# Kernel optimization log

Hardware: AMD Instinct MI355X
Metric: run time of the kernel (lower is better)

The kernel has to match this reference:

```python
import jax, jax.numpy as jnp
import numpy as np

B, T, IN = 8, 1000, 80
CONV = 256
CCEP = 222            # ltv_out_channels
FFT_SIZE = 1024
HOP = 256
WIN = 2 * HOP         # 512
PAD = (FFT_SIZE - CCEP) // 2   # 401
NFFT = 2048


def _conv1d_same(x, W, b, groups):
    # x: (B,T,C); W: (O, C//groups, 3); equivalent to torch Conv1d pad=2 then [1:-1]
    y = jax.lax.conv_general_dilated(
        jnp.transpose(x, (0, 2, 1)), W, (1,), [(1, 1)],
        feature_group_count=groups,
        dimension_numbers=('NCH', 'OIH', 'NCH'))
    return jnp.transpose(y, (0, 2, 1)) + b


def _forward(x, z, W1, b1, W2, b2, W3, b3, W4, b4):
    Bx, Tx, _ = x.shape
    # ---- ConvLayers ----
    h = jax.nn.relu(_conv1d_same(x, W1, b1, 1))
    h = jax.nn.relu(_conv1d_same(h, W2, b2, 8))
    h = jax.nn.relu(_conv1d_same(h, W3, b3, 8))
    ccep = _conv1d_same(h, W4, b4, 1)            # (B,T,222)
    q = jnp.arange(1, CCEP // 2 + 1, dtype=x.dtype)
    quef = jnp.concatenate([q[::-1], q])          # [111..1,1..111]
    ccep = ccep / quef
    # ---- ccep -> impulse (log-magnitude cepstrum -> minimum-ish phase impulse) ----
    c = jnp.pad(ccep, ((0, 0), (0, 0), (PAD, PAD)))           # (B,T,1024)
    Y = jnp.fft.fft(c, n=FFT_SIZE, axis=-1)
    mag = jnp.power(10.0, Y.real)
    imp = jnp.fft.ifft(mag * jnp.exp(1j * Y.imag), n=FFT_SIZE, axis=-1).real  # (B,T,1024)
    # ---- time-varying impulse convolution (cross-correlation per frame) ----
    L = z.shape[-1]
    zz = z.reshape(Bx, 1, L)
    zp = jnp.pad(zz, ((0, 0), (0, 0), (WIN // 2 - 1, WIN // 2)))
    starts = jnp.arange(Tx) * HOP
    frames = zp[:, :, starts[:, None] + jnp.arange(WIN)]       # (B,1,T,512)
    fp = jnp.pad(frames, ((0, 0), (0, 0), (0, 0), (FFT_SIZE // 2 - 1, FFT_SIZE // 2)))  # len 1535
    # corr[s] = sum_k fp[s+k] * imp[k], s in [0,512); linear corr via zero-padded FFT
    Fz = jnp.fft.rfft(fp, n=NFFT, axis=-1)                     # (B,1,T,NFFT//2+1)
    Fy = jnp.fft.rfft(imp, n=NFFT, axis=-1)[:, None]           # (B,1,T,NFFT//2+1)
    corr = jnp.fft.irfft(Fz * jnp.conj(Fy), n=NFFT, axis=-1)[..., :WIN]  # (B,1,T,512)
    # ---- overlap-add ----
    n = jnp.arange(WIN, dtype=x.dtype)
    win = 0.5 * (1.0 - jnp.cos(2.0 * jnp.pi * n / WIN))        # periodic hann, win_norm=1
    zw = corr * win
    l, r = zw[..., :HOP], zw[..., HOP:]
    out = l + jnp.roll(r, 1, axis=2)
    return out.reshape(Bx, 1, Tx * HOP)


def setup_inputs() -> dict:
    key = jax.random.key(0)
    ks = jax.random.split(key, 12)
    x = jax.random.normal(ks[0], (B, T, IN), dtype=jnp.float32)
    z = jax.random.normal(ks[1], (B, 1, T * HOP), dtype=jnp.float32)
    def w(k, o, i, kk, scale):
        return jax.random.normal(k, (o, i, kk), dtype=jnp.float32) * (scale / np.sqrt(i * kk))
    W1 = w(ks[2], CONV, IN, 3, 1.0)
    b1 = jnp.zeros((CONV,), jnp.float32)
    W2 = w(ks[3], CONV, CONV // 8, 3, 1.0)
    b2 = jnp.zeros((CONV,), jnp.float32)
    W3 = w(ks[4], CONV, CONV // 8, 3, 1.0)
    b3 = jnp.zeros((CONV,), jnp.float32)
    W4 = w(ks[5], CCEP, CONV, 3, 0.01)   # small scale keeps 10**(.) well-conditioned
    b4 = jnp.zeros((CCEP,), jnp.float32)
    return {"x": x, "z": z, "W1": W1, "b1": b1, "W2": W2, "b2": b2,
            "W3": W3, "b3": b3, "W4": W4, "b4": b4}


def reference(x, z, W1, b1, W2, b2, W3, b3, W4, b4):
    return _forward(x, z, W1, b1, W2, b2, W3, b3, W4, b4)
```

## Files before the change

kernel.cpp:

```cpp
#include <hip/hip_runtime.h>
#include <hip/hip_bf16.h>

#define T_LEN 1000
#define B_N 8
#define IN_CH 80
#define CONV_CH 256
#define CCEP_N 222

typedef short s8v __attribute__((ext_vector_type(8)));
typedef float f16v __attribute__((ext_vector_type(16)));

#define TWO_PI 6.28318530717958647692f

__global__ __launch_bounds__(256) void k_prep(
    const float* __restrict__ W1, const float* __restrict__ W2,
    const float* __restrict__ W3, const float* __restrict__ W4,
    float* __restrict__ Wt1, float* __restrict__ Wt2, float* __restrict__ Wt3,
    __hip_bfloat16* __restrict__ Wc, float2* __restrict__ twTab,
    float* __restrict__ winTab) {
  const int bid = blockIdx.x, tid = threadIdx.x;
  if (bid < 240) {
    int e = bid * 256 + tid;
    int o = e / 240, k = e - o * 240;
    Wt1[k * 256 + o] = W1[e];
  } else if (bid < 336) {
    int e = (bid - 240) * 256 + tid;
    int o = e / 96, k = e - o * 96;
    Wt2[k * 256 + o] = W2[e];
  } else if (bid < 432) {
    int e = (bid - 336) * 256 + tid;
    int o = e / 96, k = e - o * 96;
    Wt3[k * 256 + o] = W3[e];
  } else if (bid < 1200) {
    int e = (bid - 432) * 256 + tid;
    int kloc = e & 31, n = (e >> 5) & 255, chg = e >> 13;
    int kp = chg * 32 + kloc;
    int kappa = kp >> 8, i = kp & 255;
    float v = 0.f;
    if (n < CCEP_N) {
      float invq = 1.f / (float)((n < 111) ? (111 - n) : (n - 110));
      v = W4[n * 768 + i * 3 + kappa] * invq;
    }
    Wc[e] = __float2bfloat16(v);
  } else {
    int e = (bid - 1200) * 256 + tid;
    if (e < 1020) {
      int Q, off;
      if (e < 768)       { Q = 256; off = 0; }
      else if (e < 960)  { Q = 64;  off = 768; }
      else if (e < 1008) { Q = 16;  off = 960; }
      else               { Q = 4;   off = 1008; }
      int rem = e - off;
      int r = rem / Q, pos = rem - r * Q;
      float ang = (TWO_PI * (float)((r + 1) * pos)) / (float)(4 * Q);
      float s, c;
      sincosf(ang, &s, &c);
      twTab[e] = make_float2(c, s);
    } else if (e < 1532) {
      int n = e - 1020;
      winTab[n] = (0.5f - 0.5f * cosf(TWO_PI * (float)n / 512.f)) * (1.f / 1024.f);
    }
  }
}

__global__ __launch_bounds__(256) void k_conv1t(const float* __restrict__ x,
    const float* __restrict__ Wt, const float* __restrict__ bias,
    float* __restrict__ out) {
  const int b = blockIdx.y;
  const int t0 = blockIdx.x * 10;
  const int o = threadIdx.x;
  __shared__ float hs[IN_CH * 14];
  for (int e = threadIdx.x; e < 12 * IN_CH; e += 256) {
    int r = e / IN_CH, c = e - r * IN_CH;
    int t = t0 - 1 + r;
    hs[c * 14 + r] = (t >= 0 && t < T_LEN) ? x[(b * T_LEN + t) * IN_CH + c] : 0.f;
  }
  __syncthreads();
  float acc[10];
  float bv = bias[o];
#pragma unroll
  for (int j = 0; j < 10; j++) acc[j] = bv;
  for (int i = 0; i < IN_CH; i++) {
    float w0 = Wt[(3 * i + 0) * 256 + o];
    float w1 = Wt[(3 * i + 1) * 256 + o];
    float w2 = Wt[(3 * i + 2) * 256 + o];
    const float* row = &hs[i * 14];
    float a[12];
#pragma unroll
    for (int u = 0; u < 6; u++) *(float2*)&a[2 * u] = *(const float2*)(row + 2 * u);
#pragma unroll
    for (int j = 0; j < 10; j++) {
      acc[j] = fmaf(a[j], w0, acc[j]);
      acc[j] = fmaf(a[j + 1], w1, acc[j]);
      acc[j] = fmaf(a[j + 2], w2, acc[j]);
    }
  }
#pragma unroll
  for (int j = 0; j < 10; j++)
    out[(b * T_LEN + t0 + j) * CONV_CH + o] = fmaxf(acc[j], 0.f);
}

__global__ __launch_bounds__(256) void k_convg2(const float* __restrict__ h,
    const float* __restrict__ Wt2, const float* __restrict__ b2,
    const float* __restrict__ Wt3, const float* __restrict__ b3,
    __hip_bfloat16* __restrict__ out) {
  const int b = blockIdx.y;
  const int t0 = blockIdx.x * 10;
  const int o = threadIdx.x;
  const int cb = (o >> 5) << 5;
  __shared__ float hs1[CONV_CH * 14];
  __shared__ float hs2[CONV_CH * 14];
  for (int e = threadIdx.x; e < 14 * CONV_CH; e += 256) {
    int r = e >> 8, c = e & 255;
    int t = t0 - 2 + r;
    hs1[c * 14 + r] = (t >= 0 && t < T_LEN) ? h[(b * T_LEN + t) * CONV_CH + c] : 0.f;
  }
  __syncthreads();
  {
    float acc[12];
    float bv = b2[o];
#pragma unroll
    for (int j = 0; j < 12; j++) acc[j] = bv;
    for (int i = 0; i < 32; i++) {
      float w0 = Wt2[(3 * i + 0) * 256 + o];
      float w1 = Wt2[(3 * i + 1) * 256 + o];
      float w2 = Wt2[(3 * i + 2) * 256 + o];
      const float* row = &hs1[(cb + i) * 14];
      float a[14];
#pragma unroll
      for (int u = 0; u < 7; u++) *(float2*)&a[2 * u] = *(const float2*)(row + 2 * u);
#pragma unroll
      for (int j = 0; j < 12; j++) {
        acc[j] = fmaf(a[j], w0, acc[j]);
        acc[j] = fmaf(a[j + 1], w1, acc[j]);
        acc[j] = fmaf(a[j + 2], w2, acc[j]);
      }
    }
#pragma unroll
    for (int j = 0; j < 12; j++) {
      int t = t0 - 1 + j;
      hs2[o * 14 + j] = (t >= 0 && t < T_LEN) ? fmaxf(acc[j], 0.f) : 0.f;
    }
  }
  __syncthreads();
  {
    float acc[10];
    float bv = b3[o];
#pragma unroll
    for (int j = 0; j < 10; j++) acc[j] = bv;
    for (int i = 0; i < 32; i++) {
      float w0 = Wt3[(3 * i + 0) * 256 + o];
      float w1 = Wt3[(3 * i + 1) * 256 + o];
      float w2 = Wt3[(3 * i + 2) * 256 + o];
      const float* row = &hs2[(cb + i) * 14];
      float a[12];
#pragma unroll
      for (int u = 0; u < 6; u++) *(float2*)&a[2 * u] = *(const float2*)(row + 2 * u);
#pragma unroll
      for (int j = 0; j < 10; j++) {
        acc[j] = fmaf(a[j], w0, acc[j]);
        acc[j] = fmaf(a[j + 1], w1, acc[j]);
        acc[j] = fmaf(a[j + 2], w2, acc[j]);
      }
    }
#pragma unroll
    for (int j = 0; j < 10; j++)
      out[(b * T_LEN + t0 + j) * CONV_CH + o] = __float2bfloat16(fmaxf(acc[j], 0.f));
  }
}

#define APITCH 264
#define BPITCH 40
#define PSTRIDE 1792000
__global__ __launch_bounds__(256) void k_conv4m(
    const __hip_bfloat16* __restrict__ h3, const __hip_bfloat16* __restrict__ Wc,
    const float* __restrict__ bias, float* __restrict__ Pbase) {
  const int mb = blockIdx.x, b = blockIdx.y, ks = blockIdx.z;
  float* __restrict__ P = Pbase + (size_t)ks * PSTRIDE;
  const int t0 = mb * 64;
  const int tid = threadIdx.x;
  const int w = tid >> 6, lane = tid & 63;
  const int wm = w >> 1, wn = w & 1;
  const int lm = lane & 31, half = lane >> 5;

  __shared__ short h3s[67 * APITCH];
  __shared__ short Bs[2][256 * BPITCH];

  const ushort* h3u = (const ushort*)h3;
  for (int g = tid; g < 67 * 64; g += 256) {
    int rr = g >> 6, c4 = g & 63;
    int t = t0 + rr - 1;
    uint2 v = make_uint2(0u, 0u);
    if (t >= 0 && t < T_LEN)
      v = *(const uint2*)(h3u + (b * T_LEN + t) * CONV_CH + c4 * 4);
    *(uint2*)(h3s + rr * APITCH + c4 * 4) = v;
  }

  const ushort* Wu = (const ushort*)(Wc) + (size_t)(ks * 6) * 8192;
#pragma unroll
  for (int it = 0; it < 4; ++it) {
    int idx = (it * 256 + tid) * 8;
    uint4 v = *(const uint4*)(Wu + idx);
    int n = idx >> 5, kloc = idx & 31;
    *(uint4*)(Bs[0] + n * BPITCH + kloc) = v;
  }
  __syncthreads();

  f16v acc0 = {}, acc1 = {}, acc2 = {}, acc3 = {};

  for (int ch = 0; ch < 6; ++ch) {
    const int p = ch & 1;
    if (ch < 5) {
      const ushort* src = Wu + (ch + 1) * 8192;
#pragma unroll
      for (int it = 0; it < 4; ++it) {
        int idx = (it * 256 + tid) * 8;
        uint4 v = *(const uint4*)(src + idx);
        int n = idx >> 5, kloc = idx & 31;
        *(uint4*)(Bs[p ^ 1] + n * BPITCH + kloc) = v;
      }
    }
#pragma unroll
    for (int s = 0; s < 2; ++s) {
      int k0 = ks * 192 + ch * 32 + s * 16;
      int kappa = k0 >> 8, i0 = k0 & 255;
      s8v a = *(const s8v*)(h3s + (wm * 32 + lm + kappa) * APITCH + i0 + half * 8);
      const short* bp = Bs[p] + (wn * 128 + lm) * BPITCH + s * 16 + half * 8;
      s8v b0 = *(const s8v*)(bp);
      s8v b1 = *(const s8v*)(bp + 32 * BPITCH);
      s8v b2 = *(const s8v*)(bp + 64 * BPITCH);
      s8v b3 = *(const s8v*)(bp + 96 * BPITCH);
      acc0 = __builtin_amdgcn_mfma_f32_32x32x16_bf16(a, b0, acc0, 0, 0, 0);
      acc1 = __builtin_amdgcn_mfma_f32_32x32x16_bf16(a, b1, acc1, 0, 0, 0);
      acc2 = __builtin_amdgcn_mfma_f32_32x32x16_bf16(a, b2, acc2, 0, 0, 0);
      acc3 = __builtin_amdgcn_mfma_f32_32x32x16_bf16(a, b3, acc3, 0, 0, 0);
    }
    __syncthreads();
  }

  const int col = lm;
#pragma unroll
  for (int nt = 0; nt < 4; ++nt) {
    int c = wn * 128 + nt * 32 + col;
    if (c >= CCEP_N) continue;
    float bq = 0.f;
    if (ks == 0) {
      float invq = 1.f / (float)((c < 111) ? (111 - c) : (c - 110));
      bq = bias[c] * invq;
    }
    const f16v* A = (nt == 0) ? &acc0 : (nt == 1) ? &acc1 : (nt == 2) ? &acc2 : &acc3;
#pragma unroll
    for (int reg = 0; reg < 16; ++reg) {
      int row = (reg & 3) + 8 * (reg >> 2) + 4 * half;
      int t = t0 + wm * 32 + row;
      if (t < T_LEN)
        P[(size_t)(b * T_LEN + t) * 224 + c] = (*A)[reg] + bq;
    }
  }
}

__device__ __forceinline__ float2 cmul(float2 a, float2 b) {
  return make_float2(fmaf(a.x, b.x, -(a.y * b.y)), fmaf(a.x, b.y, a.y * b.x));
}
__device__ __forceinline__ float2 cadd(float2 a, float2 b) { return make_float2(a.x + b.x, a.y + b.y); }
__device__ __forceinline__ float2 csub(float2 a, float2 b) { return make_float2(a.x - b.x, a.y - b.y); }

#define LIDX(i) ((i) + ((i) >> 2))

template <int Q, int OFF>
__device__ __forceinline__ void fwd_stage2(float2* __restrict__ A,
    float2* __restrict__ B, const float2* __restrict__ Tw, int j) {
  const int pos = j & (Q - 1);
  const int base = ((j - pos) << 2) + pos;
  float2 e1 = Tw[OFF + pos], e2 = Tw[OFF + Q + pos], e3 = Tw[OFF + 2 * Q + pos];
  const float2 w1 = make_float2(e1.x, -e1.y);
  const float2 w2 = make_float2(e2.x, -e2.y);
  const float2 w3 = make_float2(e3.x, -e3.y);
#pragma unroll
  for (int arr = 0; arr < 2; ++arr) {
    float2* X = arr ? B : A;
    float2 a = X[LIDX(base)], b = X[LIDX(base + Q)];
    float2 cc = X[LIDX(base + 2 * Q)], d = X[LIDX(base + 3 * Q)];
    float2 t0 = cadd(a, cc), t1 = csub(a, cc), t2 = cadd(b, d), bd = csub(b, d);
    float2 t3 = make_float2(bd.y, -bd.x);
    X[LIDX(base)]         = cadd(t0, t2);
    X[LIDX(base + Q)]     = cmul(cadd(t1, t3), w1);
    X[LIDX(base + 2 * Q)] = cmul(csub(t0, t2), w2);
    X[LIDX(base + 3 * Q)] = cmul(csub(t1, t3), w3);
  }
}

template <int Q, int OFF>
__device__ __forceinline__ void inv_stage_t(float2* __restrict__ X,
    const float2* __restrict__ Tw, int j) {
  const int pos = j & (Q - 1);
  const int base = ((j - pos) << 2) + pos;
  const float2 w1 = Tw[OFF + pos];
  const float2 w2 = Tw[OFF + Q + pos];
  const float2 w3 = Tw[OFF + 2 * Q + pos];
  float2 a = X[LIDX(base)];
  float2 b = cmul(X[LIDX(base + Q)], w1);
  float2 cc = cmul(X[LIDX(base + 2 * Q)], w2);
  float2 d = cmul(X[LIDX(base + 3 * Q)], w3);
  float2 t0 = cadd(a, cc), t1 = csub(a, cc), t2 = cadd(b, d), bd = csub(b, d);
  float2 t3 = make_float2(-bd.y, bd.x);
  X[LIDX(base)]         = cadd(t0, t2);
  X[LIDX(base + Q)]     = cadd(t1, t3);
  X[LIDX(base + 2 * Q)] = csub(t0, t2);
  X[LIDX(base + 3 * Q)] = csub(t1, t3);
}

__device__ __forceinline__ int rev4d(int v) {
  return ((v & 3) << 6) | (((v >> 2) & 3) << 4) | (((v >> 4) & 3) << 2) | ((v >> 6) & 3);
}

__global__ __launch_bounds__(256) void k_fft(const float* __restrict__ Pb,
    const float* __restrict__ z, const float2* __restrict__ twg,
    const float* __restrict__ wing, float* __restrict__ out,
    float* __restrict__ sbl, float* __restrict__ sbr) {
  const int u = blockIdx.x, b = blockIdx.y;
  const int tA = 2 * u, tB = tA + 1;
  const int btA = b * T_LEN + tA, btB = btA + 1;
  const int j = threadIdx.x;
  __shared__ float2 WlA[1280];
  __shared__ float2 WlB[1280];
  __shared__ float2 Tws[1020];
  for (int e = j; e < 1020; e += 256) Tws[e] = twg[e];

  const float* zb = z + b * 256000;
  float f0A = 0.f, fS, f1B = 0.f;
  {
    int zi0 = tA * 256 + j - 255;
    f0A = (zi0 >= 0) ? zb[zi0] : 0.f;
    fS = zb[tA * 256 + j + 1];
    int zi2 = tB * 256 + j + 1;
    f1B = (zi2 < 256000) ? zb[zi2] : 0.f;
  }
  float c1A = 0.f, c2A = 0.f, c1B = 0.f, c2B = 0.f;
  if (j >= 145) {
    int mA = btA * 224 + (j - 145), mB = btB * 224 + (j - 145);
    c1A = (Pb[mA] + Pb[mA + PSTRIDE]) + (Pb[mA + 2 * PSTRIDE] + Pb[mA + 3 * PSTRIDE]);
    c1B = (Pb[mB] + Pb[mB + PSTRIDE]) + (Pb[mB + 2 * PSTRIDE] + Pb[mB + 3 * PSTRIDE]);
  }
  if (j < 111) {
    int mA = btA * 224 + (j + 111), mB = btB * 224 + (j + 111);
    c2A = (Pb[mA] + Pb[mA + PSTRIDE]) + (Pb[mA + 2 * PSTRIDE] + Pb[mA + 3 * PSTRIDE]);
    c2B = (Pb[mB] + Pb[mB + PSTRIDE]) + (Pb[mB + 2 * PSTRIDE] + Pb[mB + 3 * PSTRIDE]);
  }
  __syncthreads();

  {
    float2 e1 = Tws[j], e2 = Tws[256 + j], e3 = Tws[512 + j];
    const float2 w1 = make_float2(e1.x, -e1.y);
    const float2 w2 = make_float2(e2.x, -e2.y);
    const float2 w3 = make_float2(e3.x, -e3.y);
    {
      float2 t0 = make_float2(c2A, f0A);
      float2 t1 = make_float2(-c2A, f0A);
      float2 t2 = make_float2(c1A, fS);
      float2 t3 = make_float2(fS, -c1A);
      WlA[LIDX(j)]       = cadd(t0, t2);
      WlA[LIDX(j + 256)] = cmul(cadd(t1, t3), w1);
      WlA[LIDX(j + 512)] = cmul(csub(t0, t2), w2);
      WlA[LIDX(j + 768)] = cmul(csub(t1, t3), w3);
    }
    {
      float2 t0 = make_float2(c2B, fS);
      float2 t1 = make_float2(-c2B, fS);
      float2 t2 = make_float2(c1B, f1B);
      float2 t3 = make_float2(f1B, -c1B);
      WlB[LIDX(j)]       = cadd(t0, t2);
      WlB[LIDX(j + 256)] = cmul(cadd(t1, t3), w1);
      WlB[LIDX(j + 512)] = cmul(csub(t0, t2), w2);
      WlB[LIDX(j + 768)] = cmul(csub(t1, t3), w3);
    }
  }
  __syncthreads();

  fwd_stage2<64, 768>(WlA, WlB, Tws, j);  __syncthreads();
  fwd_stage2<16, 960>(WlA, WlB, Tws, j);  __syncthreads();
  fwd_stage2<4, 1008>(WlA, WlB, Tws, j);  __syncthreads();

  const int base = 4 * j;
  float2 XA[4], XB[4];
  {
    float2 u0 = WlA[LIDX(base)], u1 = WlA[LIDX(base + 1)];
    float2 u2 = WlA[LIDX(base + 2)], u3 = WlA[LIDX(base + 3)];
    float2 t0 = cadd(u0, u2), t1 = csub(u0, u2), t2 = cadd(u1, u3), bd = csub(u1, u3);
    float2 t3 = make_float2(bd.y, -bd.x);
    XA[0] = cadd(t0, t2); XA[1] = cadd(t1, t3); XA[2] = csub(t0, t2); XA[3] = csub(t1, t3);
  }
  {
    float2 u0 = WlB[LIDX(base)], u1 = WlB[LIDX(base + 1)];
    float2 u2 = WlB[LIDX(base + 2)], u3 = WlB[LIDX(base + 3)];
    float2 t0 = cadd(u0, u2), t1 = csub(u0, u2), t2 = cadd(u1, u3), bd = csub(u1, u3);
    float2 t3 = make_float2(bd.y, -bd.x);
    XB[0] = cadd(t0, t2); XB[1] = cadd(t1, t3); XB[2] = csub(t0, t2); XB[3] = csub(t1, t3);
  }
#pragma unroll
  for (int q = 0; q < 4; ++q) { WlA[LIDX(base + q)] = XA[q]; WlB[LIDX(base + q)] = XB[q]; }
  __syncthreads();

  const int r0 = rev4d(j);
  const bool self0 = (r0 == 0);
  const int jp = self0 ? 0 : rev4d((256 - r0) & 255);
  float2 PA[4], PB[4];
#pragma unroll
  for (int q = 0; q < 4; ++q) { PA[q] = WlA[LIDX(4 * jp + q)]; PB[q] = WlB[LIDX(4 * jp + q)]; }
  float2 Z[4];
#pragma unroll
  for (int q = 0; q < 4; ++q) {
    float2 SA, SB;
    {
      float2 A = XA[q];
      float2 Bc = self0 ? PA[(4 - q) & 3] : PA[3 - q];
      float2 Y = make_float2(0.5f * (A.x + Bc.x), 0.5f * (A.y - Bc.y));
      float2 F = make_float2(0.5f * (A.y + Bc.y), -0.5f * (A.x - Bc.x));
      float mag = __expf(Y.x * 2.30258509299404568402f);
      float sy, cy;
      __sincosf(Y.y, &sy, &cy);
      float gr = mag * cy, gi = mag * sy;
      SA = make_float2(fmaf(F.x, gr, F.y * gi), fmaf(F.x, gi, -(F.y * gr)));
    }
    {
      float2 A = XB[q];
      float2 Bc = self0 ? PB[(4 - q) & 3] : PB[3 - q];
      float2 Y = make_float2(0.5f * (A.x + Bc.x), 0.5f * (A.y - Bc.y));
      float2 F = make_float2(0.5f * (A.y + Bc.y), -0.5f * (A.x - Bc.x));
      float mag = __expf(Y.x * 2.30258509299404568402f);
      float sy, cy;
      __sincosf(Y.y, &sy, &cy);
      float gr = mag * cy, gi = mag * sy;
      SB = make_float2(fmaf(F.x, gr, F.y * gi), fmaf(F.x, gi, -(F.y * gr)));
    }
    Z[q] = make_float2(SA.x - SB.y, SA.y + SB.x);
  }
  __syncthreads();

  {
    float2 t0 = cadd(Z[0], Z[2]), t1 = csub(Z[0], Z[2]), t2 = cadd(Z[1], Z[3]), bd = csub(Z[1], Z[3]);
    float2 t3 = make_float2(-bd.y, bd.x);
    WlA[LIDX(base)]     = cadd(t0, t2);
    WlA[LIDX(base + 1)] = cadd(t1, t3);
    WlA[LIDX(base + 2)] = csub(t0, t2);
    WlA[LIDX(base + 3)] = csub(t1, t3);
  }
  __syncthreads();

  inv_stage_t<4, 1008>(WlA, Tws, j);  __syncthreads();
  inv_stage_t<16, 960>(WlA, Tws, j);  __syncthreads();
  inv_stage_t<64, 768>(WlA, Tws, j);  __syncthreads();

  {
    float2 w1 = Tws[j], w2 = Tws[256 + j], w3 = Tws[512 + j];
    float2 a = WlA[LIDX(j)];
    float2 bb = cmul(WlA[LIDX(j + 256)], w1);
    float2 cc = cmul(WlA[LIDX(j + 512)], w2);
    float2 d = cmul(WlA[LIDX(j + 768)], w3);
    float2 t0 = cadd(a, cc), t1 = csub(a, cc), t2 = cadd(bb, d), bd = csub(bb, d);
    float2 t3 = make_float2(-bd.y, bd.x);
    float2 Cj    = cadd(t0, t2);
    float2 Cj256 = cadd(t1, t3);
    int n1 = 511 - j, n2 = 255 - j;
    float wn1 = wing[n1], wn2 = wing[n2];
    float vA_l = Cj256.x * wn2;
    float vAB  = Cj.x * wn1 + Cj256.y * wn2;
    float vB_r = Cj.y * wn1;
    out[(b * T_LEN + tB) * 256 + n2] = vAB;
    int su = (b * 500 + u) * 256 + n2;
    sbl[su] = vA_l;
    sbr[su] = vB_r;
  }
}

__global__ __launch_bounds__(256) void k_even(const float* __restrict__ sbl,
    const float* __restrict__ sbr, float* __restrict__ out) {
  int idx = blockIdx.x * 256 + threadIdx.x;
  int n = idx & 255;
  int bu = idx >> 8;
  int u = bu % 500, b = bu / 500;
  int up = (u == 0) ? 499 : u - 1;
  out[(b * T_LEN + 2 * u) * 256 + n] = sbl[idx] + sbr[(b * 500 + up) * 256 + n];
}

extern "C" void kernel_launch(void* const* d_in, const int* in_sizes, int n_in,
                              void* d_out, int out_size, void* d_ws, size_t ws_size,
                              hipStream_t stream) {
  const float* x  = (const float*)d_in[0];
  const float* z  = (const float*)d_in[1];
  const float* W1 = (const float*)d_in[2];
  const float* b1 = (const float*)d_in[3];
  const float* W2 = (const float*)d_in[4];
  const float* b2 = (const float*)d_in[5];
  const float* W3 = (const float*)d_in[6];
  const float* b3 = (const float*)d_in[7];
  const float* W4 = (const float*)d_in[8];
  const float* b4 = (const float*)d_in[9];

  float* ws   = (float*)d_ws;
  float* bufA = ws;
  __hip_bfloat16* h3bf = (__hip_bfloat16*)(ws + 2048000);
  float* Pb   = ws + 3072000;
  float* sbl  = ws + 10240000;
  float* sbr  = ws + 11264000;
  float* Wt1  = ws + 12288000;
  float* Wt2  = ws + 12349440;
  float* Wt3  = ws + 12374016;
  __hip_bfloat16* Wc = (__hip_bfloat16*)(ws + 12398592);
  float2* twTab = (float2*)(ws + 12496896);
  float* winTab = ws + 12498944;
  float* out = (float*)d_out;

  dim3 blk(256);
  k_prep<<<1206, blk, 0, stream>>>(W1, W2, W3, W4, Wt1, Wt2, Wt3, Wc,
                                   twTab, winTab);

  dim3 cgrid10(T_LEN / 10, B_N);
  k_conv1t<<<cgrid10, blk, 0, stream>>>(x, Wt1, b1, bufA);
  k_convg2<<<cgrid10, blk, 0, stream>>>(bufA, Wt2, b2, Wt3, b3, h3bf);
  dim3 g4(16, B_N, 4);
  k_conv4m<<<g4, blk, 0, stream>>>(h3bf, Wc, b4, Pb);
  dim3 gf(T_LEN / 2, B_N);
  k_fft<<<gf, blk, 0, stream>>>(Pb, z, twTab, winTab, out, sbl, sbr);
  k_even<<<4000, blk, 0, stream>>>(sbl, sbr, out);
}
```

Measured before the change: 173.4 us.

## Fuse first convolution into grouped conv kernel with halo recompute

Merges the first dense conv layer into the kernel that runs the two grouped convs. Each block now loads a wider input window and recomputes conv1 for 14 time steps into shared memory. This removes the intermediate fp32 activation buffer's global write and read and one kernel launch. In exchange it adds redundant halo computation for conv1 and more shared memory per block.

```diff
diff --git a/kernel.cpp b/kernel.cpp
--- a/kernel.cpp
+++ b/kernel.cpp
@@ -63,44 +63,8 @@
   }
 }
 
-__global__ __launch_bounds__(256) void k_conv1t(const float* __restrict__ x,
-    const float* __restrict__ Wt, const float* __restrict__ bias,
-    float* __restrict__ out) {
-  const int b = blockIdx.y;
-  const int t0 = blockIdx.x * 10;
-  const int o = threadIdx.x;
-  __shared__ float hs[IN_CH * 14];
-  for (int e = threadIdx.x; e < 12 * IN_CH; e += 256) {
-    int r = e / IN_CH, c = e - r * IN_CH;
-    int t = t0 - 1 + r;
-    hs[c * 14 + r] = (t >= 0 && t < T_LEN) ? x[(b * T_LEN + t) * IN_CH + c] : 0.f;
-  }
-  __syncthreads();
-  float acc[10];
-  float bv = bias[o];
-#pragma unroll
-  for (int j = 0; j < 10; j++) acc[j] = bv;
-  for (int i = 0; i < IN_CH; i++) {
-    float w0 = Wt[(3 * i + 0) * 256 + o];
-    float w1 = Wt[(3 * i + 1) * 256 + o];
-    float w2 = Wt[(3 * i + 2) * 256 + o];
-    const float* row = &hs[i * 14];
-    float a[12];
-#pragma unroll
-    for (int u = 0; u < 6; u++) *(float2*)&a[2 * u] = *(const float2*)(row + 2 * u);
-#pragma unroll
-    for (int j = 0; j < 10; j++) {
-      acc[j] = fmaf(a[j], w0, acc[j]);
-      acc[j] = fmaf(a[j + 1], w1, acc[j]);
-      acc[j] = fmaf(a[j + 2], w2, acc[j]);
-    }
-  }
-#pragma unroll
-  for (int j = 0; j < 10; j++)
-    out[(b * T_LEN + t0 + j) * CONV_CH + o] = fmaxf(acc[j], 0.f);
-}
-
-__global__ __launch_bounds__(256) void k_convg2(const float* __restrict__ h,
+__global__ __launch_bounds__(256) void k_convall(const float* __restrict__ x,
+    const float* __restrict__ Wt1, const float* __restrict__ b1,
     const float* __restrict__ Wt2, const float* __restrict__ b2,
     const float* __restrict__ Wt3, const float* __restrict__ b3,
     __hip_bfloat16* __restrict__ out) {
@@ -108,12 +72,40 @@
   const int t0 = blockIdx.x * 10;
   const int o = threadIdx.x;
   const int cb = (o >> 5) << 5;
+  __shared__ float xs[IN_CH * 18];
   __shared__ float hs1[CONV_CH * 14];
   __shared__ float hs2[CONV_CH * 14];
-  for (int e = threadIdx.x; e < 14 * CONV_CH; e += 256) {
-    int r = e >> 8, c = e & 255;
-    int t = t0 - 2 + r;
-    hs1[c * 14 + r] = (t >= 0 && t < T_LEN) ? h[(b * T_LEN + t) * CONV_CH + c] : 0.f;
+  for (int e = threadIdx.x; e < 16 * IN_CH; e += 256) {
+    int r = e / IN_CH, c = e - r * IN_CH;
+    int t = t0 - 3 + r;
+    xs[c * 18 + r] = (t >= 0 && t < T_LEN) ? x[(b * T_LEN + t) * IN_CH + c] : 0.f;
+  }
+  __syncthreads();
+  {
+    float acc[14];
+    float bv = b1[o];
+#pragma unroll
+    for (int j = 0; j < 14; j++) acc[j] = bv;
+    for (int i = 0; i < IN_CH; i++) {
+      float w0 = Wt1[(3 * i + 0) * 256 + o];
+      float w1 = Wt1[(3 * i + 1) * 256 + o];
+      float w2 = Wt1[(3 * i + 2) * 256 + o];
+      const float* row = &xs[i * 18];
+      float a[16];
+#pragma unroll
+      for (int u = 0; u < 8; u++) *(float2*)&a[2 * u] = *(const float2*)(row + 2 * u);
+#pragma unroll
+      for (int j = 0; j < 14; j++) {
+        acc[j] = fmaf(a[j], w0, acc[j]);
+        acc[j] = fmaf(a[j + 1], w1, acc[j]);
+        acc[j] = fmaf(a[j + 2], w2, acc[j]);
+      }
+    }
+#pragma unroll
+    for (int j = 0; j < 14; j++) {
+      int t = t0 - 2 + j;
+      hs1[o * 14 + j] = (t >= 0 && t < T_LEN) ? fmaxf(acc[j], 0.f) : 0.f;
+    }
   }
   __syncthreads();
   {
@@ -136,6 +128,7 @@
         acc[j] = fmaf(a[j + 2], w2, acc[j]);
       }
     }
+    __syncthreads();
 #pragma unroll
     for (int j = 0; j < 12; j++) {
       int t = t0 - 1 + j;
@@ -498,17 +491,16 @@
   const float* b4 = (const float*)d_in[9];
 
   float* ws   = (float*)d_ws;
-  float* bufA = ws;
-  __hip_bfloat16* h3bf = (__hip_bfloat16*)(ws + 2048000);
-  float* Pb   = ws + 3072000;
-  float* sbl  = ws + 10240000;
-  float* sbr  = ws + 11264000;
-  float* Wt1  = ws + 12288000;
-  float* Wt2  = ws + 12349440;
-  float* Wt3  = ws + 12374016;
-  __hip_bfloat16* Wc = (__hip_bfloat16*)(ws + 12398592);
-  float2* twTab = (float2*)(ws + 12496896);
-  float* winTab = ws + 12498944;
+  __hip_bfloat16* h3bf = (__hip_bfloat16*)ws;
+  float* Pb   = ws + 1024000;
+  float* sbl  = ws + 8192000;
+  float* sbr  = ws + 9216000;
+  float* Wt1  = ws + 10240000;
+  float* Wt2  = ws + 10301440;
+  float* Wt3  = ws + 10326016;
+  __hip_bfloat16* Wc = (__hip_bfloat16*)(ws + 10350592);
+  float2* twTab = (float2*)(ws + 10448896);
+  float* winTab = ws + 10450944;
   float* out = (float*)d_out;
 
   dim3 blk(256);
@@ -516,8 +508,7 @@
                                    twTab, winTab);
 
   dim3 cgrid10(T_LEN / 10, B_N);
-  k_conv1t<<<cgrid10, blk, 0, stream>>>(x, Wt1, b1, bufA);
-  k_convg2<<<cgrid10, blk, 0, stream>>>(bufA, Wt2, b2, Wt3, b3, h3bf);
+  k_convall<<<cgrid10, blk, 0, stream>>>(x, Wt1, b1, Wt2, b2, Wt3, b3, h3bf);
   dim3 g4(16, B_N, 4);
   k_conv4m<<<g4, blk, 0, stream>>>(h3bf, Wc, b4, Pb);
   dim3 gf(T_LEN / 2, B_N);
```

New measurement: 172.9 us (median of 2 runs). Within noise of the previous version (-0.3%).
